# Optimization experiments

Measured on AMD Instinct MI355X. Metric: run time of the kernel, lower is better.

The kernel has to match this reference:

```python
import jax, jax.numpy as jnp
import numpy as np

D_X = 1024
D_TEXT = 768
FUSION_DIM = D_X + D_TEXT  # 1792
M = 16
K = 2


def setup_inputs() -> dict:
    key = jax.random.key(0)
    k1, k2, k3, k4, k5 = jax.random.split(key, 5)
    B, H, W = 256, 32, 32
    x = jax.random.normal(k1, (B, D_X, H, W), dtype=jnp.float32)
    degraded = jax.random.normal(k2, (B, D_TEXT), dtype=jnp.float32)
    # learned params (random so routing is non-trivial)
    w_fusion = jax.random.normal(k3, (FUSION_DIM, FUSION_DIM), dtype=jnp.float32) * (1.0 / np.sqrt(FUSION_DIM))
    b_fusion = jax.random.normal(k4, (FUSION_DIM,), dtype=jnp.float32) * 0.01
    w_gate = jax.random.normal(k5, (FUSION_DIM, M), dtype=jnp.float32) * 0.02
    return {"x": x, "degraded": degraded, "w_fusion": w_fusion,
            "b_fusion": b_fusion, "w_gate": w_gate}


def reference(x, degraded, w_fusion, b_fusion, w_gate):
    B = x.shape[0]
    # global average pool over H,W -> [B, d_x]
    x_pooled = jnp.mean(x, axis=(2, 3))
    fused = jnp.concatenate([x_pooled, degraded], axis=1)        # [B, d_x+d_text]
    fused = jnp.dot(fused, w_fusion) + b_fusion                  # Linear
    fused = jax.nn.gelu(fused, approximate=False)                # exact GELU (torch default)
    clean_logits = jnp.dot(fused, w_gate)                        # [B, M]
    probs_for_mi = jax.nn.softmax(clean_logits, axis=1)
    # eval path: logits = clean_logits (no noise)
    num_consider = min(K + 1, M)
    top_logits, top_indices = jax.lax.top_k(clean_logits, num_consider)
    top_k_logits = top_logits[:, :K]
    top_k_indices = top_indices[:, :K]
    top_k_gates = jax.nn.softmax(top_k_logits, axis=1)
    rows = jnp.arange(B)[:, None]
    gates = jnp.zeros_like(clean_logits).at[rows, top_k_indices].set(top_k_gates)
    moe_loss = jnp.float32(0.0)
    return gates, moe_loss, probs_for_mi, top_k_indices
```

## Files before the change

### kernel.cpp

```cpp
#include <hip/hip_runtime.h>
#include <math.h>

#define D_X      1024
#define D_TEXT   768
#define FDIM     1792
#define BATCH    256
#define M_EXP    16
#define HW_TOT   1024

#define OUT_GATES 0
#define OUT_LOSS  4096
#define OUT_PROBS 4097
#define OUT_IDX   8193

#define POOL_BLOCKS 2048
#define NROWS (BATCH * D_X)

__global__ __launch_bounds__(256) void pool_copy_kernel(const float* __restrict__ x,
                                                        const float* __restrict__ deg,
                                                        float* __restrict__ fused) {
    const int tid  = threadIdx.x;
    const int lane = tid & 63;
    const int gw   = blockIdx.x * 4 + (tid >> 6);

    for (int r2 = gw * 2; r2 < NROWS; r2 += 2 * 4 * POOL_BLOCKS) {
        const float4* x0 = reinterpret_cast<const float4*>(x + (size_t)r2 * HW_TOT);
        float4 v0[4], v1[4];
#pragma unroll
        for (int k = 0; k < 4; ++k) v0[k] = x0[k * 64 + lane];
#pragma unroll
        for (int k = 0; k < 4; ++k) v1[k] = x0[256 + k * 64 + lane];
        float s0 = 0.0f, s1 = 0.0f;
#pragma unroll
        for (int k = 0; k < 4; ++k) {
            s0 += v0[k].x + v0[k].y + v0[k].z + v0[k].w;
            s1 += v1[k].x + v1[k].y + v1[k].z + v1[k].w;
        }
#pragma unroll
        for (int off = 32; off > 0; off >>= 1) {
            s0 += __shfl_xor(s0, off, 64);
            s1 += __shfl_xor(s1, off, 64);
        }
        if (lane == 0) {
            const int b = r2 >> 10;
            const int c = r2 & 1023;
            float2 st;
            st.x = s0 * (1.0f / 1024.0f);
            st.y = s1 * (1.0f / 1024.0f);
            *reinterpret_cast<float2*>(&fused[(size_t)b * FDIM + c]) = st;
        }
    }

    for (int id = blockIdx.x * 256 + tid; id < BATCH * (D_TEXT / 4); id += POOL_BLOCKS * 256) {
        const int b  = id / (D_TEXT / 4);
        const int j4 = id % (D_TEXT / 4);
        reinterpret_cast<float4*>(fused)[(size_t)b * (FDIM / 4) + (D_X / 4) + j4] =
            reinterpret_cast<const float4*>(deg)[id];
    }
}

#define BM 32
#define BN 64
#define BK 32
#define KSPLIT 2
#define KPB (FDIM / KSPLIT)
#define NIT (KPB / BK)

#define LOADA(k0)                                                                         \
    pa[0] = *reinterpret_cast<const float4*>(A + (size_t)(m0 + ar) * FDIM + (k0) + ak4);  \
    pa[1] = *reinterpret_cast<const float4*>(A + (size_t)(m0 + ar + 16) * FDIM + (k0) + ak4);

#define LOADW(k0)                                                                              \
    pw[0] = *reinterpret_cast<const float4*>(W + (size_t)((k0) + wr) * FDIM + n0 + wc4);       \
    pw[1] = *reinterpret_cast<const float4*>(W + (size_t)((k0) + wr + 8) * FDIM + n0 + wc4);   \
    pw[2] = *reinterpret_cast<const float4*>(W + (size_t)((k0) + wr + 16) * FDIM + n0 + wc4);  \
    pw[3] = *reinterpret_cast<const float4*>(W + (size_t)((k0) + wr + 24) * FDIM + n0 + wc4);

#define STOREA(b)                                                                 \
    As[b][ak4 + 0][ar] = pa[0].x; As[b][ak4 + 1][ar] = pa[0].y;                   \
    As[b][ak4 + 2][ar] = pa[0].z; As[b][ak4 + 3][ar] = pa[0].w;                   \
    As[b][ak4 + 0][ar + 16] = pa[1].x; As[b][ak4 + 1][ar + 16] = pa[1].y;         \
    As[b][ak4 + 2][ar + 16] = pa[1].z; As[b][ak4 + 3][ar + 16] = pa[1].w;

#define STOREW(b)                                                                 \
    *reinterpret_cast<float4*>(&Ws[b][wr][wc4])      = pw[0];                     \
    *reinterpret_cast<float4*>(&Ws[b][wr + 8][wc4])  = pw[1];                     \
    *reinterpret_cast<float4*>(&Ws[b][wr + 16][wc4]) = pw[2];                     \
    *reinterpret_cast<float4*>(&Ws[b][wr + 24][wc4]) = pw[3];

__global__ __launch_bounds__(128) void gemm_split_kernel(const float* __restrict__ A,
                                                         const float* __restrict__ W,
                                                         float* __restrict__ pact) {
    __shared__ float As[2][BK][BM + 4];
    __shared__ float Ws[2][BK][BN];

    const int tid = threadIdx.x;
    const int tx  = tid & 15;
    const int ty  = tid >> 4;
    const int m0  = blockIdx.x * BM;
    const int n0  = blockIdx.y * BN;
    const int kz  = blockIdx.z * KPB;

    const int ar  = tid >> 3;
    const int ak4 = (tid & 7) * 4;
    const int wr  = tid >> 4;
    const int wc4 = (tid & 15) * 4;

    float4 pa[2], pw[4];

    LOADA(kz); LOADW(kz);
    STOREA(0); STOREW(0);
    LOADA(kz + BK); LOADW(kz + BK);
    __syncthreads();

    float acc[4][4] = {};
    int cur = 0;

    for (int t = 0; t < NIT; ++t) {
#pragma unroll
        for (int kk = 0; kk < BK; ++kk) {
            const float4 a = *reinterpret_cast<const float4*>(&As[cur][kk][ty * 4]);
            const float4 w = *reinterpret_cast<const float4*>(&Ws[cur][kk][tx * 4]);
            const float av[4] = {a.x, a.y, a.z, a.w};
            const float wv[4] = {w.x, w.y, w.z, w.w};
#pragma unroll
            for (int i = 0; i < 4; ++i)
#pragma unroll
                for (int j = 0; j < 4; ++j)
                    acc[i][j] = fmaf(av[i], wv[j], acc[i][j]);
        }
        if (t < NIT - 1) {
            const int nxt = cur ^ 1;
            STOREA(nxt); STOREW(nxt);
            if (t < NIT - 2) {
                const int k0 = kz + (t + 2) * BK;
                LOADA(k0); LOADW(k0);
            }
            __syncthreads();
            cur = nxt;
        }
    }

    float* o = pact + ((size_t)blockIdx.z * BATCH + m0 + ty * 4) * FDIM + n0 + tx * 4;
#pragma unroll
    for (int i = 0; i < 4; ++i) {
        float4 v;
        v.x = acc[i][0]; v.y = acc[i][1]; v.z = acc[i][2]; v.w = acc[i][3];
        *reinterpret_cast<float4*>(o + (size_t)i * FDIM) = v;
    }
}

__global__ __launch_bounds__(256) void reduce_gate_kernel(const float* __restrict__ pact,
                                                          const float* __restrict__ bias,
                                                          const float* __restrict__ wg,
                                                          float* __restrict__ part) {
    __shared__ float actS[BM][BN + 1];
    __shared__ float wgs[BN][M_EXP];

    const int tid = threadIdx.x;
    const int m0 = blockIdx.x * BM;
    const int n0 = blockIdx.y * BN;

    {
        const int r  = tid >> 2;
        const int c4 = (tid & 3) * 4;
        *reinterpret_cast<float4*>(&wgs[r][c4]) =
            *reinterpret_cast<const float4*>(wg + (size_t)(n0 + r) * M_EXP + c4);
    }

    const int row = tid >> 3;
    const int c8  = (tid & 7) * 8;
    const size_t base = (size_t)(m0 + row) * FDIM + n0 + c8;
#pragma unroll
    for (int h = 0; h < 2; ++h) {
        const float4 p0 = *reinterpret_cast<const float4*>(pact + base + h * 4);
        const float4 p1 = *reinterpret_cast<const float4*>(pact + (size_t)BATCH * FDIM + base + h * 4);
        const float4 bb = *reinterpret_cast<const float4*>(bias + n0 + c8 + h * 4);
        const float vv[4] = {p0.x + p1.x + bb.x, p0.y + p1.y + bb.y,
                             p0.z + p1.z + bb.z, p0.w + p1.w + bb.w};
#pragma unroll
        for (int j = 0; j < 4; ++j)
            actS[row][c8 + h * 4 + j] =
                vv[j] * 0.5f * (1.0f + erff(vv[j] * 0.70710678118654752440f));
    }
    __syncthreads();

    const int pm = tid >> 3;
    const int pe = (tid & 7) * 2;
    float s0 = 0.0f, s1 = 0.0f;
#pragma unroll
    for (int n = 0; n < BN; ++n) {
        const float a = actS[pm][n];
        s0 = fmaf(a, wgs[n][pe], s0);
        s1 = fmaf(a, wgs[n][pe + 1], s1);
    }
    float* pr = part + ((size_t)blockIdx.y * BATCH + m0 + pm) * M_EXP + pe;
    pr[0] = s0;
    pr[1] = s1;
}

#define NNB (FDIM / BN)

__global__ __launch_bounds__(64) void finalize_kernel(const float* __restrict__ part,
                                                      float* __restrict__ out) {
    const int b = blockIdx.x * 64 + threadIdx.x;

    float l[M_EXP];
#pragma unroll
    for (int m = 0; m < M_EXP; ++m) l[m] = 0.0f;

    for (int nb = 0; nb < NNB; ++nb) {
        const float4* pr = reinterpret_cast<const float4*>(part + ((size_t)nb * BATCH + b) * M_EXP);
#pragma unroll
        for (int q = 0; q < 4; ++q) {
            const float4 v = pr[q];
            l[q * 4 + 0] += v.x;
            l[q * 4 + 1] += v.y;
            l[q * 4 + 2] += v.z;
            l[q * 4 + 3] += v.w;
        }
    }

    float mx = l[0];
#pragma unroll
    for (int m = 1; m < M_EXP; ++m) mx = fmaxf(mx, l[m]);
    float e[M_EXP], s = 0.0f;
#pragma unroll
    for (int m = 0; m < M_EXP; ++m) { e[m] = expf(l[m] - mx); s += e[m]; }
    const float inv = 1.0f / s;
#pragma unroll
    for (int m = 0; m < M_EXP; ++m) out[OUT_PROBS + b * M_EXP + m] = e[m] * inv;

    int i0 = 0; float v0 = l[0];
#pragma unroll
    for (int m = 1; m < M_EXP; ++m) if (l[m] > v0) { v0 = l[m]; i0 = m; }
    int i1 = -1; float v1 = -INFINITY;
#pragma unroll
    for (int m = 0; m < M_EXP; ++m) if (m != i0 && l[m] > v1) { v1 = l[m]; i1 = m; }

    const float t = expf(v1 - v0);
    const float g0 = 1.0f / (1.0f + t);
    const float g1 = t * g0;

#pragma unroll
    for (int m = 0; m < M_EXP; ++m) out[OUT_GATES + b * M_EXP + m] = 0.0f;
    out[OUT_GATES + b * M_EXP + i0] = g0;
    out[OUT_GATES + b * M_EXP + i1] = g1;

    out[OUT_IDX + b * 2 + 0] = (float)i0;
    out[OUT_IDX + b * 2 + 1] = (float)i1;

    if (b == 0) out[OUT_LOSS] = 0.0f;
}

extern "C" void kernel_launch(void* const* d_in, const int* in_sizes, int n_in,
                              void* d_out, int out_size, void* d_ws, size_t ws_size,
                              hipStream_t stream) {
    const float* x        = (const float*)d_in[0];
    const float* degraded = (const float*)d_in[1];
    const float* w_fusion = (const float*)d_in[2];
    const float* b_fusion = (const float*)d_in[3];
    const float* w_gate   = (const float*)d_in[4];
    float* out = (float*)d_out;

    float* fused = (float*)d_ws;
    float* pact  = fused + (size_t)BATCH * FDIM;
    float* part  = pact + (size_t)KSPLIT * BATCH * FDIM;

    pool_copy_kernel<<<POOL_BLOCKS, 256, 0, stream>>>(x, degraded, fused);

    gemm_split_kernel<<<dim3(BATCH / BM, FDIM / BN, KSPLIT), 128, 0, stream>>>(fused, w_fusion, pact);

    reduce_gate_kernel<<<dim3(BATCH / BM, FDIM / BN), 256, 0, stream>>>(pact, b_fusion, w_gate, part);

    finalize_kernel<<<BATCH / 64, 64, 0, stream>>>(part, out);
}
```

Before: 288.0 us.

## Enlarge GEMM tiles to 128x128 with 8-way split-K and flatten pooling grid

The fusion GEMM moves from 32x64 tiles with 128 threads and split-K 2 to 128x128 tiles with 256 threads, 8x8 register blocking and split-K 8. The aim is more data reuse per shared-memory load and enough blocks to fill the device. The cost is eight partial buffers the reduce kernel must now sum, which adds memory traffic. The pooling kernel is also rewritten to launch one wave per row with a separate set of blocks for the text copy, replacing the grid-stride loop.

```diff
diff --git a/kernel.cpp b/kernel.cpp
--- a/kernel.cpp
+++ b/kernel.cpp
@@ -13,62 +13,54 @@
 #define OUT_PROBS 4097
 #define OUT_IDX   8193
 
-#define POOL_BLOCKS 2048
-#define NROWS (BATCH * D_X)
+#define NBLK_POOL (BATCH * D_X / 4)
+#define NBLK_COPY 192
 
 __global__ __launch_bounds__(256) void pool_copy_kernel(const float* __restrict__ x,
                                                         const float* __restrict__ deg,
                                                         float* __restrict__ fused) {
-    const int tid  = threadIdx.x;
-    const int lane = tid & 63;
-    const int gw   = blockIdx.x * 4 + (tid >> 6);
-
-    for (int r2 = gw * 2; r2 < NROWS; r2 += 2 * 4 * POOL_BLOCKS) {
-        const float4* x0 = reinterpret_cast<const float4*>(x + (size_t)r2 * HW_TOT);
-        float4 v0[4], v1[4];
-#pragma unroll
-        for (int k = 0; k < 4; ++k) v0[k] = x0[k * 64 + lane];
-#pragma unroll
-        for (int k = 0; k < 4; ++k) v1[k] = x0[256 + k * 64 + lane];
-        float s0 = 0.0f, s1 = 0.0f;
+    const int blk = blockIdx.x;
+    if (blk < NBLK_POOL) {
+        const int gtid = blk * 256 + threadIdx.x;
+        const int row  = gtid >> 6;
+        const int lane = gtid & 63;
+        const float4* xr = reinterpret_cast<const float4*>(x + (size_t)row * HW_TOT);
+        float s = 0.0f;
 #pragma unroll
         for (int k = 0; k < 4; ++k) {
-            s0 += v0[k].x + v0[k].y + v0[k].z + v0[k].w;
-            s1 += v1[k].x + v1[k].y + v1[k].z + v1[k].w;
-        }
-#pragma unroll
-        for (int off = 32; off > 0; off >>= 1) {
-            s0 += __shfl_xor(s0, off, 64);
-            s1 += __shfl_xor(s1, off, 64);
-        }
+            float4 v = xr[k * 64 + lane];
+            s += v.x + v.y + v.z + v.w;
+        }
+#pragma unroll
+        for (int off = 32; off > 0; off >>= 1) s += __shfl_xor(s, off, 64);
         if (lane == 0) {
-            const int b = r2 >> 10;
-            const int c = r2 & 1023;
-            float2 st;
-            st.x = s0 * (1.0f / 1024.0f);
-            st.y = s1 * (1.0f / 1024.0f);
-            *reinterpret_cast<float2*>(&fused[(size_t)b * FDIM + c]) = st;
-        }
-    }
-
-    for (int id = blockIdx.x * 256 + tid; id < BATCH * (D_TEXT / 4); id += POOL_BLOCKS * 256) {
-        const int b  = id / (D_TEXT / 4);
-        const int j4 = id % (D_TEXT / 4);
-        reinterpret_cast<float4*>(fused)[(size_t)b * (FDIM / 4) + (D_X / 4) + j4] =
-            reinterpret_cast<const float4*>(deg)[id];
-    }
-}
-
-#define BM 32
-#define BN 64
+            const int b = row >> 10;
+            const int c = row & 1023;
+            fused[(size_t)b * FDIM + c] = s * (1.0f / 1024.0f);
+        }
+    } else {
+        const int tid = (blk - NBLK_POOL) * 256 + threadIdx.x;
+        if (tid < BATCH * (D_TEXT / 4)) {
+            const int b  = tid / (D_TEXT / 4);
+            const int j4 = tid % (D_TEXT / 4);
+            const float4 v = reinterpret_cast<const float4*>(deg)[tid];
+            reinterpret_cast<float4*>(fused)[(size_t)b * (FDIM / 4) + (D_X / 4) + j4] = v;
+        }
+    }
+}
+
+#define TM 128
+#define TN 128
 #define BK 32
-#define KSPLIT 2
-#define KPB (FDIM / KSPLIT)
-#define NIT (KPB / BK)
-
-#define LOADA(k0)                                                                         \
-    pa[0] = *reinterpret_cast<const float4*>(A + (size_t)(m0 + ar) * FDIM + (k0) + ak4);  \
-    pa[1] = *reinterpret_cast<const float4*>(A + (size_t)(m0 + ar + 16) * FDIM + (k0) + ak4);
+#define KSPLIT 8
+#define KCH (FDIM / KSPLIT)
+#define NIT (KCH / BK)
+
+#define LOADA(k0)                                                                              \
+    pa[0] = *reinterpret_cast<const float4*>(A + (size_t)(m0 + ar) * FDIM + (k0) + ak4);       \
+    pa[1] = *reinterpret_cast<const float4*>(A + (size_t)(m0 + ar + 32) * FDIM + (k0) + ak4);  \
+    pa[2] = *reinterpret_cast<const float4*>(A + (size_t)(m0 + ar + 64) * FDIM + (k0) + ak4);  \
+    pa[3] = *reinterpret_cast<const float4*>(A + (size_t)(m0 + ar + 96) * FDIM + (k0) + ak4);
 
 #define LOADW(k0)                                                                              \
     pw[0] = *reinterpret_cast<const float4*>(W + (size_t)((k0) + wr) * FDIM + n0 + wc4);       \
@@ -77,10 +69,13 @@
     pw[3] = *reinterpret_cast<const float4*>(W + (size_t)((k0) + wr + 24) * FDIM + n0 + wc4);
 
 #define STOREA(b)                                                                 \
-    As[b][ak4 + 0][ar] = pa[0].x; As[b][ak4 + 1][ar] = pa[0].y;                   \
-    As[b][ak4 + 2][ar] = pa[0].z; As[b][ak4 + 3][ar] = pa[0].w;                   \
-    As[b][ak4 + 0][ar + 16] = pa[1].x; As[b][ak4 + 1][ar + 16] = pa[1].y;         \
-    As[b][ak4 + 2][ar + 16] = pa[1].z; As[b][ak4 + 3][ar + 16] = pa[1].w;
+    _Pragma("unroll")                                                             \
+    for (int q = 0; q < 4; ++q) {                                                 \
+        As[b][ak4 + q][ar]      = ((const float*)&pa[0])[q];                      \
+        As[b][ak4 + q][ar + 32] = ((const float*)&pa[1])[q];                      \
+        As[b][ak4 + q][ar + 64] = ((const float*)&pa[2])[q];                      \
+        As[b][ak4 + q][ar + 96] = ((const float*)&pa[3])[q];                      \
+    }
 
 #define STOREW(b)                                                                 \
     *reinterpret_cast<float4*>(&Ws[b][wr][wc4])      = pw[0];                     \
@@ -88,45 +83,47 @@
     *reinterpret_cast<float4*>(&Ws[b][wr + 16][wc4]) = pw[2];                     \
     *reinterpret_cast<float4*>(&Ws[b][wr + 24][wc4]) = pw[3];
 
-__global__ __launch_bounds__(128) void gemm_split_kernel(const float* __restrict__ A,
+__global__ __launch_bounds__(256) void gemm_split_kernel(const float* __restrict__ A,
                                                          const float* __restrict__ W,
                                                          float* __restrict__ pact) {
-    __shared__ float As[2][BK][BM + 4];
-    __shared__ float Ws[2][BK][BN];
+    __shared__ float As[2][BK][TM];
+    __shared__ float Ws[2][BK][TN];
 
     const int tid = threadIdx.x;
     const int tx  = tid & 15;
     const int ty  = tid >> 4;
-    const int m0  = blockIdx.x * BM;
-    const int n0  = blockIdx.y * BN;
-    const int kz  = blockIdx.z * KPB;
+    const int m0  = blockIdx.x * TM;
+    const int n0  = blockIdx.y * TN;
+    const int kz  = blockIdx.z * KCH;
 
     const int ar  = tid >> 3;
     const int ak4 = (tid & 7) * 4;
-    const int wr  = tid >> 4;
-    const int wc4 = (tid & 15) * 4;
-
-    float4 pa[2], pw[4];
+    const int wr  = tid >> 5;
+    const int wc4 = (tid & 31) * 4;
+
+    float4 pa[4], pw[4];
 
     LOADA(kz); LOADW(kz);
     STOREA(0); STOREW(0);
     LOADA(kz + BK); LOADW(kz + BK);
     __syncthreads();
 
-    float acc[4][4] = {};
+    float acc[8][8] = {};
     int cur = 0;
 
     for (int t = 0; t < NIT; ++t) {
 #pragma unroll
         for (int kk = 0; kk < BK; ++kk) {
-            const float4 a = *reinterpret_cast<const float4*>(&As[cur][kk][ty * 4]);
-            const float4 w = *reinterpret_cast<const float4*>(&Ws[cur][kk][tx * 4]);
-            const float av[4] = {a.x, a.y, a.z, a.w};
-            const float wv[4] = {w.x, w.y, w.z, w.w};
-#pragma unroll
-            for (int i = 0; i < 4; ++i)
-#pragma unroll
-                for (int j = 0; j < 4; ++j)
+            const float4 a0 = *reinterpret_cast<const float4*>(&As[cur][kk][ty * 4]);
+            const float4 a1 = *reinterpret_cast<const float4*>(&As[cur][kk][64 + ty * 4]);
+            const float4 w0 = *reinterpret_cast<const float4*>(&Ws[cur][kk][tx * 4]);
+            const float4 w1 = *reinterpret_cast<const float4*>(&Ws[cur][kk][64 + tx * 4]);
+            const float av[8] = {a0.x, a0.y, a0.z, a0.w, a1.x, a1.y, a1.z, a1.w};
+            const float wv[8] = {w0.x, w0.y, w0.z, w0.w, w1.x, w1.y, w1.z, w1.w};
+#pragma unroll
+            for (int i = 0; i < 8; ++i)
+#pragma unroll
+                for (int j = 0; j < 8; ++j)
                     acc[i][j] = fmaf(av[i], wv[j], acc[i][j]);
         }
         if (t < NIT - 1) {
@@ -141,25 +138,31 @@
         }
     }
 
-    float* o = pact + ((size_t)blockIdx.z * BATCH + m0 + ty * 4) * FDIM + n0 + tx * 4;
-#pragma unroll
-    for (int i = 0; i < 4; ++i) {
-        float4 v;
-        v.x = acc[i][0]; v.y = acc[i][1]; v.z = acc[i][2]; v.w = acc[i][3];
-        *reinterpret_cast<float4*>(o + (size_t)i * FDIM) = v;
-    }
-}
+#pragma unroll
+    for (int i = 0; i < 8; ++i) {
+        const int m = m0 + ((i < 4) ? (ty * 4 + i) : (64 + ty * 4 + (i - 4)));
+        float* o = pact + ((size_t)blockIdx.z * BATCH + m) * FDIM + n0;
+        float4 v0, v1;
+        v0.x = acc[i][0]; v0.y = acc[i][1]; v0.z = acc[i][2]; v0.w = acc[i][3];
+        v1.x = acc[i][4]; v1.y = acc[i][5]; v1.z = acc[i][6]; v1.w = acc[i][7];
+        *reinterpret_cast<float4*>(o + tx * 4)      = v0;
+        *reinterpret_cast<float4*>(o + 64 + tx * 4) = v1;
+    }
+}
+
+#define BM2 32
+#define BN2 64
 
 __global__ __launch_bounds__(256) void reduce_gate_kernel(const float* __restrict__ pact,
                                                           const float* __restrict__ bias,
                                                           const float* __restrict__ wg,
                                                           float* __restrict__ part) {
-    __shared__ float actS[BM][BN + 1];
-    __shared__ float wgs[BN][M_EXP];
+    __shared__ float actS[BM2][BN2 + 1];
+    __shared__ float wgs[BN2][M_EXP];
 
     const int tid = threadIdx.x;
-    const int m0 = blockIdx.x * BM;
-    const int n0 = blockIdx.y * BN;
+    const int m0 = blockIdx.x * BM2;
+    const int n0 = blockIdx.y * BN2;
 
     {
         const int r  = tid >> 2;
@@ -173,11 +176,14 @@
     const size_t base = (size_t)(m0 + row) * FDIM + n0 + c8;
 #pragma unroll
     for (int h = 0; h < 2; ++h) {
-        const float4 p0 = *reinterpret_cast<const float4*>(pact + base + h * 4);
-        const float4 p1 = *reinterpret_cast<const float4*>(pact + (size_t)BATCH * FDIM + base + h * 4);
         const float4 bb = *reinterpret_cast<const float4*>(bias + n0 + c8 + h * 4);
-        const float vv[4] = {p0.x + p1.x + bb.x, p0.y + p1.y + bb.y,
-                             p0.z + p1.z + bb.z, p0.w + p1.w + bb.w};
+        float vv[4] = {bb.x, bb.y, bb.z, bb.w};
+#pragma unroll
+        for (int z = 0; z < KSPLIT; ++z) {
+            const float4 p = *reinterpret_cast<const float4*>(
+                pact + (size_t)z * BATCH * FDIM + base + h * 4);
+            vv[0] += p.x; vv[1] += p.y; vv[2] += p.z; vv[3] += p.w;
+        }
 #pragma unroll
         for (int j = 0; j < 4; ++j)
             actS[row][c8 + h * 4 + j] =
@@ -189,7 +195,7 @@
     const int pe = (tid & 7) * 2;
     float s0 = 0.0f, s1 = 0.0f;
 #pragma unroll
-    for (int n = 0; n < BN; ++n) {
+    for (int n = 0; n < BN2; ++n) {
         const float a = actS[pm][n];
         s0 = fmaf(a, wgs[n][pe], s0);
         s1 = fmaf(a, wgs[n][pe + 1], s1);
@@ -199,7 +205,7 @@
     pr[1] = s1;
 }
 
-#define NNB (FDIM / BN)
+#define NNB (FDIM / BN2)
 
 __global__ __launch_bounds__(64) void finalize_kernel(const float* __restrict__ part,
                                                       float* __restrict__ out) {
@@ -267,11 +273,11 @@
     float* pact  = fused + (size_t)BATCH * FDIM;
     float* part  = pact + (size_t)KSPLIT * BATCH * FDIM;
 
-    pool_copy_kernel<<<POOL_BLOCKS, 256, 0, stream>>>(x, degraded, fused);
-
-    gemm_split_kernel<<<dim3(BATCH / BM, FDIM / BN, KSPLIT), 128, 0, stream>>>(fused, w_fusion, pact);
-
-    reduce_gate_kernel<<<dim3(BATCH / BM, FDIM / BN), 256, 0, stream>>>(pact, b_fusion, w_gate, part);
+    pool_copy_kernel<<<NBLK_POOL + NBLK_COPY, 256, 0, stream>>>(x, degraded, fused);
+
+    gemm_split_kernel<<<dim3(BATCH / TM, FDIM / TN, KSPLIT), 256, 0, stream>>>(fused, w_fusion, pact);
+
+    reduce_gate_kernel<<<dim3(BATCH / BM2, FDIM / BN2), 256, 0, stream>>>(pact, b_fusion, w_gate, part);
 
     finalize_kernel<<<BATCH / 64, 64, 0, stream>>>(part, out);
 }
```

Measured after the change: 305.6 us. 6.1% more time.
